# Kernel optimization log

Hardware: AMD Instinct MI355X
Metric: run time of the kernel (lower is better)

## Reference

```python
import jax, jax.numpy as jnp
import numpy as np

S, B, D, H = 2048, 2, 1024, 16
DK = D // H
SCALE = 1.0 / np.sqrt(DK)


def setup_inputs() -> dict:
    key = jax.random.key(0)
    ks = jax.random.split(key, 12)
    std = 1.0 / np.sqrt(D)
    inp = {
        "query": jax.random.normal(ks[0], (S, B, D), jnp.float32),
        "key": jax.random.normal(ks[1], (S, B, D), jnp.float32),
        "value": jax.random.normal(ks[2], (S, B, D), jnp.float32),
        # causal mask [S, S, 1]; mask[i, j] = 1 iff query i may attend key j
        "mask": jnp.tril(jnp.ones((S, S), jnp.bool_))[:, :, None],
        "Wq": jax.random.normal(ks[3], (D, D), jnp.float32) * std,
        "bq": jax.random.normal(ks[4], (D,), jnp.float32) * std,
        "Wk": jax.random.normal(ks[5], (D, D), jnp.float32) * std,
        "bk": jax.random.normal(ks[6], (D,), jnp.float32) * std,
        "Wv": jax.random.normal(ks[7], (D, D), jnp.float32) * std,
        "bv": jax.random.normal(ks[8], (D,), jnp.float32) * std,
        "Wo": jax.random.normal(ks[9], (D, D), jnp.float32) * std,
        "bo": jax.random.normal(ks[10], (D,), jnp.float32) * std,
    }
    return inp


def _proj(x, W, b):
    # nn.Linear: x @ W.T + b, then split into heads -> [S, B, H, DK]
    s, bsz, _ = x.shape
    y = jnp.einsum('sbd,ed->sbe', x, W) + b
    return y.reshape(s, bsz, H, DK)


def reference(query, key, value, mask, Wq, bq, Wk, bk, Wv, bv, Wo, bo):
    q = _proj(query, Wq, bq)   # [S,B,H,DK]
    k = _proj(key, Wk, bk)
    v = _proj(value, Wv, bv)
    scores = jnp.einsum('ibhd,jbhd->ijbh', q, k) * SCALE  # [S,S,B,H]
    m = mask[:, :, :, None]  # [S,S,1,1] or [S,S,B,1]
    scores = jnp.where(m, scores, jnp.float32(-1e9))
    attn = jax.nn.softmax(scores, axis=1)
    x = jnp.einsum('ijbh,jbhd->ibhd', attn, v)  # [S,B,H,DK]
    x = x.reshape(S, B, D)
    return jnp.einsum('sbd,ed->sbe', x, Wo) + bo
```

## Files before the change

### kernel.cpp

```cpp
#include <hip/hip_runtime.h>
#include <stdint.h>

#define S_LEN 2048
#define BATCH 2
#define DMODEL 1024
#define NHEAD 16
#define DHEAD 64
#define QSCALE 0.18033688011112042f

typedef float f32x4 __attribute__((ext_vector_type(4)));
typedef float f32x16 __attribute__((ext_vector_type(16)));
typedef __bf16 bf16x8 __attribute__((ext_vector_type(8)));

#if __has_builtin(__builtin_amdgcn_exp2f)
#define EXP2(x) __builtin_amdgcn_exp2f(x)
#else
#define EXP2(x) exp2f(x)
#endif

__device__ __forceinline__ unsigned short f2bf(float f) {
  union { float f; unsigned int u; } v;
  v.f = f;
  unsigned int u = v.u;
  return (unsigned short)((u + 0x7fffu + ((u >> 16) & 1u)) >> 16);
}

__device__ __forceinline__ unsigned pk2(float lo, float hi_) {
  union { __bf16 h[2]; unsigned u; } c;
  c.h[0] = (__bf16)lo; c.h[1] = (__bf16)hi_;
  return c.u;
}

__device__ __forceinline__ void gld16(const void* g, void* l) {
  __builtin_amdgcn_global_load_lds((__attribute__((address_space(1))) void*)(g),
                                   (__attribute__((address_space(3))) void*)(l),
                                   16, 0, 0);
}

__global__ void cvt_all_kernel(const float* __restrict__ q, const float* __restrict__ k,
                               const float* __restrict__ v, const float* __restrict__ wq,
                               const float* __restrict__ wk, const float* __restrict__ wv,
                               const float* __restrict__ wosrc, unsigned short* __restrict__ xp,
                               unsigned short* __restrict__ wp, unsigned short* __restrict__ wo) {
  const int b = blockIdx.x;
  const float* src;
  unsigned short* dst;
  if (b < 12288) {
    const int z = b >> 12;
    const int local = b & 4095;
    src = (z == 0 ? q : (z == 1 ? k : v)) + (size_t)local * 1024;
    dst = xp + (size_t)z * 4194304 + (size_t)local * 1024;
  } else {
    const int z = (b - 12288) >> 10;
    const int local = (b - 12288) & 1023;
    src = (z == 0 ? wq : (z == 1 ? wk : (z == 2 ? wv : wosrc))) + (size_t)local * 1024;
    dst = (z < 3 ? wp + (size_t)z * 1048576 : wo) + (size_t)local * 1024;
  }
  const int i = threadIdx.x * 4;
  const float4 val = *(const float4*)(src + i);
  ushort4 o;
  o.x = f2bf(val.x); o.y = f2bf(val.y); o.z = f2bf(val.z); o.w = f2bf(val.w);
  *(ushort4*)(dst + i) = o;
}

template <int MODE>
__global__ __launch_bounds__(256, 2) void gemm_bt(
    const unsigned short* __restrict__ Abase,
    const unsigned short* __restrict__ Wbase,
    const float* __restrict__ bias0, const float* __restrict__ bias1,
    const float* __restrict__ bias2,
    unsigned short* __restrict__ qw, unsigned short* __restrict__ kw,
    unsigned short* __restrict__ vtw, float* __restrict__ outp) {
  constexpr int M = S_LEN * BATCH;
  constexpr int N = DMODEL;
  constexpr int K = DMODEL;
  __shared__ unsigned short At[128 * 32];
  __shared__ unsigned short Bt[128 * 32];

  const int m0 = blockIdx.x * 128;
  const int n0 = blockIdx.y * 128;
  const int z = (MODE == 0) ? blockIdx.z : 0;
  const unsigned short* A = Abase + (size_t)z * M * K;
  const unsigned short* W = Wbase + (size_t)z * N * K;
  const float* bias = (z == 0 ? bias0 : (z == 1 ? bias1 : bias2));

  const int tid = threadIdx.x;
  const int w = tid >> 6, l = tid & 63;
  const int wr = w >> 1, wc = w & 1;
  const int lr = l & 15, lg = l >> 4;

  const int srow = tid >> 2;
  const int scol = (tid & 3) * 8;

  f32x4 acc[4][4] = {};

  for (int k0 = 0; k0 < K; k0 += 32) {
    {
      const unsigned short* ga0 = A + (size_t)(m0 + srow) * K + k0 + scol;
      const unsigned short* ga1 = A + (size_t)(m0 + 64 + srow) * K + k0 + scol;
      const unsigned short* gb0 = W + (size_t)(n0 + srow) * K + k0 + scol;
      const unsigned short* gb1 = W + (size_t)(n0 + 64 + srow) * K + k0 + scol;
      char* la = (char*)At + w * 1024;
      char* lb = (char*)Bt + w * 1024;
      gld16(ga0, la);
      gld16(ga1, la + 4096);
      gld16(gb0, lb);
      gld16(gb1, lb + 4096);
    }
    __syncthreads();
    bf16x8 af[4], bfr[4];
#pragma unroll
    for (int mt = 0; mt < 4; ++mt)
      af[mt] = *(const bf16x8*)&At[(wr * 64 + mt * 16 + lr) * 32 + lg * 8];
#pragma unroll
    for (int nt = 0; nt < 4; ++nt)
      bfr[nt] = *(const bf16x8*)&Bt[(wc * 64 + nt * 16 + lr) * 32 + lg * 8];
#pragma unroll
    for (int mt = 0; mt < 4; ++mt)
#pragma unroll
      for (int nt = 0; nt < 4; ++nt)
        acc[mt][nt] = __builtin_amdgcn_mfma_f32_16x16x32_bf16(af[mt], bfr[nt], acc[mt][nt], 0, 0, 0);
    __syncthreads();
  }

#pragma unroll
  for (int mt = 0; mt < 4; ++mt) {
#pragma unroll
    for (int nt = 0; nt < 4; ++nt) {
#pragma unroll
      for (int r = 0; r < 4; ++r) {
        const int gm = m0 + wr * 64 + mt * 16 + lg * 4 + r;
        const int gn = n0 + wc * 64 + nt * 16 + lr;
        float v = acc[mt][nt][r] + bias[gn];
        if (MODE == 1) {
          outp[(size_t)gm * N + gn] = v;
        } else {
          if (z == 0) v *= QSCALE;
          const int s = gm >> 1, bb = gm & 1;
          const int h = gn >> 6, dk = gn & 63;
          const int bh = bb * NHEAD + h;
          const unsigned short bv_ = f2bf(v);
          if (z == 0)
            qw[((size_t)bh * S_LEN + s) * DHEAD + dk] = bv_;
          else if (z == 1)
            kw[((size_t)bh * S_LEN + s) * DHEAD + dk] = bv_;
          else
            vtw[((size_t)bh * DHEAD + dk) * S_LEN + s] = bv_;
        }
      }
    }
  }
}

__global__ __launch_bounds__(256) void attn_kernel(
    const unsigned short* __restrict__ qw, const unsigned short* __restrict__ kw,
    const unsigned short* __restrict__ vtw, unsigned short* __restrict__ x2) {
  __shared__ unsigned short klds[2][8192];
  __shared__ unsigned short vlds[2][8192];
  __shared__ float mlscr[2][64][2];

  const int bh = blockIdx.x;
  const int xq = blockIdx.y;
  const int bb = bh >> 4, h = bh & 15;
  const int tid = threadIdx.x;
  const int w = tid >> 6, l = tid & 63;
  const int q5 = l & 31, hi = l >> 5;
  const int pair = w >> 1, wh = w & 1;

  const size_t qkbase = (size_t)bh * S_LEN * DHEAD;
  const size_t vbase = (size_t)bh * DHEAD * S_LEN;

  const int qtA = 31 - xq, qtB = xq;
  const int nA = qtA + 1, nB = qtB + 1;
  const int nsA = (nA + 1) >> 1;
  const int nsTot = nsA + ((nB + 1) >> 1);

  auto stage = [&](int kt0, int kt1, int b) {
#pragma unroll
    for (int r = 0; r < 4; ++r) {
      const int kt = (r >= 2) ? kt1 : kt0;
      const int idx = (r * 256 + tid) & 511;
      const int row = idx >> 3;
      const int sw = (idx & 7) ^ (row & 7);
      gld16(kw + qkbase + (size_t)(kt * 64 + row) * DHEAD + sw * 8,
            (char*)&klds[b][0] + r * 4096 + w * 1024);
      gld16(vtw + vbase + (size_t)row * S_LEN + kt * 64 + sw * 8,
            (char*)&vlds[b][0] + r * 4096 + w * 1024);
    }
  };

  int qt = qtA;
  int qrow = qt * 64 + wh * 32 + q5;
  bf16x8 qf[4];
#pragma unroll
  for (int d = 0; d < 4; ++d)
    qf[d] = *(const bf16x8*)&qw[qkbase + (size_t)qrow * DHEAD + d * 16 + hi * 8];

  f32x16 oacc0, oacc1;
#pragma unroll
  for (int r = 0; r < 16; ++r) { oacc0[r] = 0.f; oacc1[r] = 0.f; }
  float mrun = -1e30f, lrun = 0.f;

  stage(0, 1, 0);
  __syncthreads();

  for (int s = 0; s < nsTot; ++s) {
    const int cur = s & 1;
    if (s + 1 < nsTot) {
      int t0, lim;
      if (s + 1 < nsA) { t0 = 2 * (s + 1); lim = nA; }
      else { t0 = 2 * (s + 1 - nsA); lim = nB; }
      const int k1 = (t0 + 1 < lim) ? t0 + 1 : lim - 1;
      stage(t0, k1, cur ^ 1);
    }

    const bool phA = (s < nsA);
    const int myt = (phA ? 2 * s : 2 * (s - nsA)) + pair;
    const int lim = phA ? nA : nB;

    if (myt < lim) {
      const int kt = myt;
      const char* kb = (const char*)&klds[cur][0] + pair * 8192;
      const char* vb = (const char*)&vlds[cur][0] + pair * 8192;

      f32x16 scA, scB;
#pragma unroll
      for (int r = 0; r < 16; ++r) { scA[r] = 0.f; scB[r] = 0.f; }
      __builtin_amdgcn_s_setprio(1);
#pragma unroll
      for (int d = 0; d < 4; ++d) {
        const int ch = (2 * d + hi) ^ (q5 & 7);
        const bf16x8 kfA = *(const bf16x8*)(kb + q5 * 128 + ch * 16);
        const bf16x8 kfB = *(const bf16x8*)(kb + (32 + q5) * 128 + ch * 16);
        scA = __builtin_amdgcn_mfma_f32_32x32x16_bf16(kfA, qf[d], scA, 0, 0, 0);
        scB = __builtin_amdgcn_mfma_f32_32x32x16_bf16(kfB, qf[d], scB, 0, 0, 0);
      }
      __builtin_amdgcn_s_setprio(0);

      if (kt == qt) {
        const int qloc = wh * 32 + q5;
#pragma unroll
        for (int r = 0; r < 16; ++r) {
          const int kv = (r & 3) + 8 * (r >> 2) + 4 * hi;
          if (kv > qloc) scA[r] = -1e9f;
          if (kv + 32 > qloc) scB[r] = -1e9f;
        }
      }

      float mx[8];
#pragma unroll
      for (int j = 0; j < 8; ++j)
        mx[j] = fmaxf(fmaxf(scA[j], scA[j + 8]), fmaxf(scB[j], scB[j + 8]));
#pragma unroll
      for (int j = 0; j < 4; ++j) mx[j] = fmaxf(mx[j], mx[j + 4]);
      float tmax = fmaxf(fmaxf(mx[0], mx[1]), fmaxf(mx[2], mx[3]));
      tmax = fmaxf(tmax, __shfl_xor(tmax, 32, 64));
      const float mnew = fmaxf(mrun, tmax);
      const float resc = EXP2(mrun - mnew);
      mrun = mnew;
#pragma unroll
      for (int r = 0; r < 16; ++r) scA[r] = EXP2(scA[r] - mnew);
#pragma unroll
      for (int r = 0; r < 16; ++r) scB[r] = EXP2(scB[r] - mnew);
      float sm[8];
#pragma unroll
      for (int j = 0; j < 8; ++j)
        sm[j] = (scA[j] + scA[j + 8]) + (scB[j] + scB[j + 8]);
#pragma unroll
      for (int j = 0; j < 4; ++j) sm[j] += sm[j + 4];
      float rsum = (sm[0] + sm[1]) + (sm[2] + sm[3]);
      rsum += __shfl_xor(rsum, 32, 64);
      lrun = lrun * resc + rsum;
#pragma unroll
      for (int r = 0; r < 16; ++r) { oacc0[r] *= resc; oacc1[r] *= resc; }

      unsigned pk[2][8];
#pragma unroll
      for (int g = 0; g < 4; ++g) {
        pk[0][2 * g]     = pk2(scA[4 * g],     scA[4 * g + 1]);
        pk[0][2 * g + 1] = pk2(scA[4 * g + 2], scA[4 * g + 3]);
        pk[1][2 * g]     = pk2(scB[4 * g],     scB[4 * g + 1]);
        pk[1][2 * g + 1] = pk2(scB[4 * g + 2], scB[4 * g + 3]);
      }

#pragma unroll
      for (int t = 0; t < 4; ++t) {
        const int c = t >> 1, ks = t & 1;
        const unsigned o0 = pk[c][4 * ks + 0], o1 = pk[c][4 * ks + 1];
        const unsigned o2 = pk[c][4 * ks + 2], o3 = pk[c][4 * ks + 3];
        const unsigned ea = (unsigned)__shfl_xor((int)(hi ? o0 : o2), 32, 64);
        const unsigned eb = (unsigned)__shfl_xor((int)(hi ? o1 : o3), 32, 64);
        union { unsigned u[4]; bf16x8 v; } pb;
        pb.u[0] = hi ? ea : o0;
        pb.u[1] = hi ? eb : o1;
        pb.u[2] = hi ? o2 : ea;
        pb.u[3] = hi ? o3 : eb;
        const int vch = (2 * t + hi) ^ (q5 & 7);
        const bf16x8 vf0 = *(const bf16x8*)(vb + q5 * 128 + vch * 16);
        const bf16x8 vf1 = *(const bf16x8*)(vb + (32 + q5) * 128 + vch * 16);
        __builtin_amdgcn_s_setprio(1);
        oacc0 = __builtin_amdgcn_mfma_f32_32x32x16_bf16(vf0, pb.v, oacc0, 0, 0, 0);
        oacc1 = __builtin_amdgcn_mfma_f32_32x32x16_bf16(vf1, pb.v, oacc1, 0, 0, 0);
        __builtin_amdgcn_s_setprio(0);
      }
    }

    if (s == nsA - 1 || s == nsTot - 1) {
      __syncthreads();
      float* scr = (float*)&klds[cur][0];
      const int kx = l & 7;
      if (pair == 1) {
        f32x4* d4 = (f32x4*)(scr + (size_t)(wh * 64 + l) * 32);
#pragma unroll
        for (int c = 0; c < 4; ++c) {
          f32x4 ch_;
#pragma unroll
          for (int j = 0; j < 4; ++j) ch_[j] = oacc0[c * 4 + j];
          d4[c ^ kx] = ch_;
        }
#pragma unroll
        for (int c = 0; c < 4; ++c) {
          f32x4 ch_;
#pragma unroll
          for (int j = 0; j < 4; ++j) ch_[j] = oacc1[c * 4 + j];
          d4[(4 + c) ^ kx] = ch_;
        }
        mlscr[wh][l][0] = mrun;
        mlscr[wh][l][1] = lrun;
      }
      __syncthreads();
      if (pair == 0) {
        const f32x4* s4 = (const f32x4*)(scr + (size_t)(wh * 64 + l) * 32);
        const float m1 = mlscr[wh][l][0], l1 = mlscr[wh][l][1];
        const float ms = fmaxf(mrun, m1);
        const float a0 = EXP2(mrun - ms), a1 = EXP2(m1 - ms);
        const float lm = lrun * a0 + l1 * a1;
        const float invl = 1.0f / lm;
        const size_t obase = ((size_t)qrow * BATCH + bb) * DMODEL + h * DHEAD;
#pragma unroll
        for (int g = 0; g < 4; ++g) {
          const f32x4 c0 = s4[g ^ kx];
          const f32x4 c1 = s4[(4 + g) ^ kx];
          ushort4 s0, s1;
          s0.x = f2bf((oacc0[4 * g + 0] * a0 + c0[0] * a1) * invl);
          s0.y = f2bf((oacc0[4 * g + 1] * a0 + c0[1] * a1) * invl);
          s0.z = f2bf((oacc0[4 * g + 2] * a0 + c0[2] * a1) * invl);
          s0.w = f2bf((oacc0[4 * g + 3] * a0 + c0[3] * a1) * invl);
          s1.x = f2bf((oacc1[4 * g + 0] * a0 + c1[0] * a1) * invl);
          s1.y = f2bf((oacc1[4 * g + 1] * a0 + c1[1] * a1) * invl);
          s1.z = f2bf((oacc1[4 * g + 2] * a0 + c1[2] * a1) * invl);
          s1.w = f2bf((oacc1[4 * g + 3] * a0 + c1[3] * a1) * invl);
          const int d0 = 8 * g + 4 * hi;
          *(ushort4*)(x2 + obase + d0) = s0;
          *(ushort4*)(x2 + obase + 32 + d0) = s1;
        }
      }
      if (s == nsA - 1) {
        qt = qtB;
        qrow = qt * 64 + wh * 32 + q5;
#pragma unroll
        for (int d = 0; d < 4; ++d)
          qf[d] = *(const bf16x8*)&qw[qkbase + (size_t)qrow * DHEAD + d * 16 + hi * 8];
#pragma unroll
        for (int r = 0; r < 16; ++r) { oacc0[r] = 0.f; oacc1[r] = 0.f; }
        mrun = -1e30f;
        lrun = 0.f;
      }
    }
    __syncthreads();
  }
}

extern "C" void kernel_launch(void* const* d_in, const int* in_sizes, int n_in,
                              void* d_out, int out_size, void* d_ws, size_t ws_size,
                              hipStream_t stream) {
  (void)in_sizes; (void)n_in; (void)out_size;
  if (ws_size < (size_t)67108864) return;

  const float* query = (const float*)d_in[0];
  const float* key_  = (const float*)d_in[1];
  const float* value = (const float*)d_in[2];
  const float* Wq = (const float*)d_in[4];
  const float* bq = (const float*)d_in[5];
  const float* Wk = (const float*)d_in[6];
  const float* bk = (const float*)d_in[7];
  const float* Wv = (const float*)d_in[8];
  const float* bv = (const float*)d_in[9];
  const float* Wo = (const float*)d_in[10];
  const float* bo = (const float*)d_in[11];

  char* ws = (char*)d_ws;
  unsigned short* xp = (unsigned short*)(ws);
  unsigned short* wp = (unsigned short*)(ws + 25165824);
  unsigned short* wo = (unsigned short*)(ws + 31457280);
  unsigned short* qws = (unsigned short*)(ws + 33554432);
  unsigned short* kws = (unsigned short*)(ws + 41943040);
  unsigned short* vtw = (unsigned short*)(ws + 50331648);
  unsigned short* x2 = (unsigned short*)(ws + 58720256);

  cvt_all_kernel<<<16384, 256, 0, stream>>>(query, key_, value, Wq, Wk, Wv, Wo, xp, wp, wo);

  gemm_bt<0><<<dim3(32, 8, 3), 256, 0, stream>>>(xp, wp, bq, bk, bv, qws, kws, vtw, nullptr);
  attn_kernel<<<dim3(32, 16), 256, 0, stream>>>(qws, kws, vtw, x2);
  gemm_bt<1><<<dim3(32, 8, 1), 256, 0, stream>>>(x2, wo, bo, bo, bo, nullptr, nullptr, nullptr,
                                                 (float*)d_out);
}
```

Before: 131.6 us.

## Fuse fp32-to-bf16 input conversion into QKV GEMM, widen attention to 8 waves

Drops the separate conversion pass over the activations: the QKV projection GEMM now loads fp32 query, key and value directly, converts them to bf16 in registers and writes a padded LDS tile, prefetching the next K-slice. The attention kernel grows to 512 threads with four key-tile groups per step, a single LDS buffer restaged after each step, and a three-way partial merge at the end. It also adds a lazy softmax rescale that skips the max update when the new max stays within 8 of the running one, and switches EXP2 to exp2f. The fused conversion saves a full read-write pass over about 50 MB of activations, but the attention kernel loses its double buffering and now waits on the restage between steps.

```diff
diff --git a/kernel.cpp b/kernel.cpp
--- a/kernel.cpp
+++ b/kernel.cpp
@@ -11,12 +11,9 @@
 typedef float f32x4 __attribute__((ext_vector_type(4)));
 typedef float f32x16 __attribute__((ext_vector_type(16)));
 typedef __bf16 bf16x8 __attribute__((ext_vector_type(8)));
-
-#if __has_builtin(__builtin_amdgcn_exp2f)
-#define EXP2(x) __builtin_amdgcn_exp2f(x)
-#else
+typedef unsigned short u16x8 __attribute__((ext_vector_type(8)));
+
 #define EXP2(x) exp2f(x)
-#endif
 
 __device__ __forceinline__ unsigned short f2bf(float f) {
   union { float f; unsigned int u; } v;
@@ -37,25 +34,13 @@
                                    16, 0, 0);
 }
 
-__global__ void cvt_all_kernel(const float* __restrict__ q, const float* __restrict__ k,
-                               const float* __restrict__ v, const float* __restrict__ wq,
-                               const float* __restrict__ wk, const float* __restrict__ wv,
-                               const float* __restrict__ wosrc, unsigned short* __restrict__ xp,
-                               unsigned short* __restrict__ wp, unsigned short* __restrict__ wo) {
+__global__ void cvt_w_kernel(const float* __restrict__ wq, const float* __restrict__ wk,
+                             const float* __restrict__ wv, const float* __restrict__ wosrc,
+                             unsigned short* __restrict__ wp, unsigned short* __restrict__ wo) {
   const int b = blockIdx.x;
-  const float* src;
-  unsigned short* dst;
-  if (b < 12288) {
-    const int z = b >> 12;
-    const int local = b & 4095;
-    src = (z == 0 ? q : (z == 1 ? k : v)) + (size_t)local * 1024;
-    dst = xp + (size_t)z * 4194304 + (size_t)local * 1024;
-  } else {
-    const int z = (b - 12288) >> 10;
-    const int local = (b - 12288) & 1023;
-    src = (z == 0 ? wq : (z == 1 ? wk : (z == 2 ? wv : wosrc))) + (size_t)local * 1024;
-    dst = (z < 3 ? wp + (size_t)z * 1048576 : wo) + (size_t)local * 1024;
-  }
+  const int z = b >> 10, local = b & 1023;
+  const float* src = (z == 0 ? wq : (z == 1 ? wk : (z == 2 ? wv : wosrc))) + (size_t)local * 1024;
+  unsigned short* dst = (z < 3 ? wp + (size_t)z * 1048576 : wo) + (size_t)local * 1024;
   const int i = threadIdx.x * 4;
   const float4 val = *(const float4*)(src + i);
   ushort4 o;
@@ -65,22 +50,22 @@
 
 template <int MODE>
 __global__ __launch_bounds__(256, 2) void gemm_bt(
-    const unsigned short* __restrict__ Abase,
+    const float* __restrict__ Aq, const float* __restrict__ Akk, const float* __restrict__ Avv,
+    const unsigned short* __restrict__ Ab,
     const unsigned short* __restrict__ Wbase,
     const float* __restrict__ bias0, const float* __restrict__ bias1,
     const float* __restrict__ bias2,
     unsigned short* __restrict__ qw, unsigned short* __restrict__ kw,
     unsigned short* __restrict__ vtw, float* __restrict__ outp) {
-  constexpr int M = S_LEN * BATCH;
   constexpr int N = DMODEL;
   constexpr int K = DMODEL;
-  __shared__ unsigned short At[128 * 32];
+  constexpr int AST = (MODE == 0) ? 40 : 32;
+  __shared__ unsigned short At[128 * AST];
   __shared__ unsigned short Bt[128 * 32];
 
   const int m0 = blockIdx.x * 128;
   const int n0 = blockIdx.y * 128;
   const int z = (MODE == 0) ? blockIdx.z : 0;
-  const unsigned short* A = Abase + (size_t)z * M * K;
   const unsigned short* W = Wbase + (size_t)z * N * K;
   const float* bias = (z == 0 ? bias0 : (z == 1 ? bias1 : bias2));
 
@@ -92,26 +77,46 @@
   const int srow = tid >> 2;
   const int scol = (tid & 3) * 8;
 
+  const int arow = tid >> 1;
+  const int aks = (tid & 1) << 4;
+  const float* Af = (MODE == 0) ? (z == 0 ? Aq : (z == 1 ? Akk : Avv)) : nullptr;
+  const float* abase = (MODE == 0) ? (Af + (size_t)(m0 + arow) * K + aks) : nullptr;
+
+  float4 av[4];
+  if (MODE == 0) {
+#pragma unroll
+    for (int c = 0; c < 4; ++c) av[c] = *(const float4*)(abase + 4 * c);
+  }
+
   f32x4 acc[4][4] = {};
 
   for (int k0 = 0; k0 < K; k0 += 32) {
-    {
-      const unsigned short* ga0 = A + (size_t)(m0 + srow) * K + k0 + scol;
-      const unsigned short* ga1 = A + (size_t)(m0 + 64 + srow) * K + k0 + scol;
-      const unsigned short* gb0 = W + (size_t)(n0 + srow) * K + k0 + scol;
-      const unsigned short* gb1 = W + (size_t)(n0 + 64 + srow) * K + k0 + scol;
-      char* la = (char*)At + w * 1024;
-      char* lb = (char*)Bt + w * 1024;
-      gld16(ga0, la);
-      gld16(ga1, la + 4096);
-      gld16(gb0, lb);
-      gld16(gb1, lb + 4096);
-    }
+    if (k0) __syncthreads();
+    if (MODE == 0) {
+      union { __bf16 h[8]; u16x8 v; } c0, c1;
+#pragma unroll
+      for (int j = 0; j < 4; ++j) { c0.h[j] = (__bf16)av[0][j]; c0.h[4 + j] = (__bf16)av[1][j]; }
+#pragma unroll
+      for (int j = 0; j < 4; ++j) { c1.h[j] = (__bf16)av[2][j]; c1.h[4 + j] = (__bf16)av[3][j]; }
+      *(u16x8*)&At[arow * AST + aks] = c0.v;
+      *(u16x8*)&At[arow * AST + aks + 8] = c1.v;
+    } else {
+      gld16(Ab + (size_t)(m0 + srow) * K + k0 + scol, (char*)At + w * 1024);
+      gld16(Ab + (size_t)(m0 + 64 + srow) * K + k0 + scol, (char*)At + w * 1024 + 4096);
+    }
+    gld16(W + (size_t)(n0 + srow) * K + k0 + scol, (char*)Bt + w * 1024);
+    gld16(W + (size_t)(n0 + 64 + srow) * K + k0 + scol, (char*)Bt + w * 1024 + 4096);
     __syncthreads();
+
+    if (MODE == 0 && k0 + 32 < K) {
+#pragma unroll
+      for (int c = 0; c < 4; ++c) av[c] = *(const float4*)(abase + k0 + 32 + 4 * c);
+    }
+
     bf16x8 af[4], bfr[4];
 #pragma unroll
     for (int mt = 0; mt < 4; ++mt)
-      af[mt] = *(const bf16x8*)&At[(wr * 64 + mt * 16 + lr) * 32 + lg * 8];
+      af[mt] = *(const bf16x8*)&At[(wr * 64 + mt * 16 + lr) * AST + lg * 8];
 #pragma unroll
     for (int nt = 0; nt < 4; ++nt)
       bfr[nt] = *(const bf16x8*)&Bt[(wc * 64 + nt * 16 + lr) * 32 + lg * 8];
@@ -120,7 +125,6 @@
 #pragma unroll
       for (int nt = 0; nt < 4; ++nt)
         acc[mt][nt] = __builtin_amdgcn_mfma_f32_16x16x32_bf16(af[mt], bfr[nt], acc[mt][nt], 0, 0, 0);
-    __syncthreads();
   }
 
 #pragma unroll
@@ -152,12 +156,11 @@
   }
 }
 
-__global__ __launch_bounds__(256) void attn_kernel(
+__global__ __launch_bounds__(512) void attn_kernel(
     const unsigned short* __restrict__ qw, const unsigned short* __restrict__ kw,
     const unsigned short* __restrict__ vtw, unsigned short* __restrict__ x2) {
-  __shared__ unsigned short klds[2][8192];
-  __shared__ unsigned short vlds[2][8192];
-  __shared__ float mlscr[2][64][2];
+  __shared__ unsigned short lds_all[32768];
+  __shared__ float mlscr[3][2][64][2];
 
   const int bh = blockIdx.x;
   const int xq = blockIdx.y;
@@ -165,27 +168,29 @@
   const int tid = threadIdx.x;
   const int w = tid >> 6, l = tid & 63;
   const int q5 = l & 31, hi = l >> 5;
-  const int pair = w >> 1, wh = w & 1;
+  const int quar = w >> 1, wh = w & 1;
 
   const size_t qkbase = (size_t)bh * S_LEN * DHEAD;
   const size_t vbase = (size_t)bh * DHEAD * S_LEN;
 
   const int qtA = 31 - xq, qtB = xq;
   const int nA = qtA + 1, nB = qtB + 1;
-  const int nsA = (nA + 1) >> 1;
-  const int nsTot = nsA + ((nB + 1) >> 1);
-
-  auto stage = [&](int kt0, int kt1, int b) {
+  const int sA = (nA + 3) >> 2;
+  const int sTot = sA + ((nB + 3) >> 2);
+
+  auto stage = [&](int t0, int lim) {
 #pragma unroll
     for (int r = 0; r < 4; ++r) {
-      const int kt = (r >= 2) ? kt1 : kt0;
-      const int idx = (r * 256 + tid) & 511;
-      const int row = idx >> 3;
-      const int sw = (idx & 7) ^ (row & 7);
-      gld16(kw + qkbase + (size_t)(kt * 64 + row) * DHEAD + sw * 8,
-            (char*)&klds[b][0] + r * 4096 + w * 1024);
-      gld16(vtw + vbase + (size_t)row * S_LEN + kt * 64 + sw * 8,
-            (char*)&vlds[b][0] + r * 4096 + w * 1024);
+      const int g = w * 4 + r;
+      const int ti = g >> 3;
+      const int row = ((g & 7) << 3) + (l >> 3);
+      const int ch = (l & 7) ^ (row & 7);
+      int t = t0 + ti;
+      if (t >= lim) t = lim - 1;
+      gld16(kw + qkbase + (size_t)(t * 64 + row) * DHEAD + ch * 8,
+            (char*)lds_all + g * 1024);
+      gld16(vtw + vbase + (size_t)row * S_LEN + t * 64 + ch * 8,
+            (char*)lds_all + 32768 + g * 1024);
     }
   };
 
@@ -201,27 +206,19 @@
   for (int r = 0; r < 16; ++r) { oacc0[r] = 0.f; oacc1[r] = 0.f; }
   float mrun = -1e30f, lrun = 0.f;
 
-  stage(0, 1, 0);
+  stage(0, nA);
   __syncthreads();
 
-  for (int s = 0; s < nsTot; ++s) {
-    const int cur = s & 1;
-    if (s + 1 < nsTot) {
-      int t0, lim;
-      if (s + 1 < nsA) { t0 = 2 * (s + 1); lim = nA; }
-      else { t0 = 2 * (s + 1 - nsA); lim = nB; }
-      const int k1 = (t0 + 1 < lim) ? t0 + 1 : lim - 1;
-      stage(t0, k1, cur ^ 1);
-    }
-
-    const bool phA = (s < nsA);
-    const int myt = (phA ? 2 * s : 2 * (s - nsA)) + pair;
+  const char* kb = (const char*)lds_all + quar * 8192;
+  const char* vb = (const char*)lds_all + 32768 + quar * 8192;
+
+  for (int s = 0; s < sTot; ++s) {
+    const bool phA = (s < sA);
+    const int myt = (phA ? 4 * s : 4 * (s - sA)) + quar;
     const int lim = phA ? nA : nB;
 
     if (myt < lim) {
       const int kt = myt;
-      const char* kb = (const char*)&klds[cur][0] + pair * 8192;
-      const char* vb = (const char*)&vlds[cur][0] + pair * 8192;
 
       f32x16 scA, scB;
 #pragma unroll
@@ -255,13 +252,18 @@
       for (int j = 0; j < 4; ++j) mx[j] = fmaxf(mx[j], mx[j + 4]);
       float tmax = fmaxf(fmaxf(mx[0], mx[1]), fmaxf(mx[2], mx[3]));
       tmax = fmaxf(tmax, __shfl_xor(tmax, 32, 64));
-      const float mnew = fmaxf(mrun, tmax);
-      const float resc = EXP2(mrun - mnew);
-      mrun = mnew;
-#pragma unroll
-      for (int r = 0; r < 16; ++r) scA[r] = EXP2(scA[r] - mnew);
-#pragma unroll
-      for (int r = 0; r < 16; ++r) scB[r] = EXP2(scB[r] - mnew);
+      if (!__all(tmax <= mrun + 8.0f)) {
+        const float mnew = fmaxf(mrun, tmax);
+        const float resc = EXP2(mrun - mnew);
+        mrun = mnew;
+        lrun *= resc;
+#pragma unroll
+        for (int r = 0; r < 16; ++r) { oacc0[r] *= resc; oacc1[r] *= resc; }
+      }
+#pragma unroll
+      for (int r = 0; r < 16; ++r) scA[r] = EXP2(scA[r] - mrun);
+#pragma unroll
+      for (int r = 0; r < 16; ++r) scB[r] = EXP2(scB[r] - mrun);
       float sm[8];
 #pragma unroll
       for (int j = 0; j < 8; ++j)
@@ -270,9 +272,7 @@
       for (int j = 0; j < 4; ++j) sm[j] += sm[j + 4];
       float rsum = (sm[0] + sm[1]) + (sm[2] + sm[3]);
       rsum += __shfl_xor(rsum, 32, 64);
-      lrun = lrun * resc + rsum;
-#pragma unroll
-      for (int r = 0; r < 16; ++r) { oacc0[r] *= resc; oacc1[r] *= resc; }
+      lrun += rsum;
 
       unsigned pk[2][8];
 #pragma unroll
@@ -305,12 +305,12 @@
       }
     }
 
-    if (s == nsA - 1 || s == nsTot - 1) {
+    if (s == sA - 1 || s == sTot - 1) {
       __syncthreads();
-      float* scr = (float*)&klds[cur][0];
+      float* scr = (float*)lds_all;
       const int kx = l & 7;
-      if (pair == 1) {
-        f32x4* d4 = (f32x4*)(scr + (size_t)(wh * 64 + l) * 32);
+      if (quar != 0) {
+        f32x4* d4 = (f32x4*)(scr + (size_t)(((quar - 1) * 2 + wh) * 64 + l) * 32);
 #pragma unroll
         for (int c = 0; c < 4; ++c) {
           f32x4 ch_;
@@ -325,37 +325,51 @@
           for (int j = 0; j < 4; ++j) ch_[j] = oacc1[c * 4 + j];
           d4[(4 + c) ^ kx] = ch_;
         }
-        mlscr[wh][l][0] = mrun;
-        mlscr[wh][l][1] = lrun;
+        mlscr[quar - 1][wh][l][0] = mrun;
+        mlscr[quar - 1][wh][l][1] = lrun;
       }
       __syncthreads();
-      if (pair == 0) {
-        const f32x4* s4 = (const f32x4*)(scr + (size_t)(wh * 64 + l) * 32);
-        const float m1 = mlscr[wh][l][0], l1 = mlscr[wh][l][1];
-        const float ms = fmaxf(mrun, m1);
-        const float a0 = EXP2(mrun - ms), a1 = EXP2(m1 - ms);
-        const float lm = lrun * a0 + l1 * a1;
+      if (quar == 0) {
+        float ms = mrun, lm = lrun;
+        f32x16 a0 = oacc0, a1 = oacc1;
+#pragma unroll
+        for (int p = 1; p <= 3; ++p) {
+          const f32x4* s4 = (const f32x4*)(scr + (size_t)(((p - 1) * 2 + wh) * 64 + l) * 32);
+          const float mp = mlscr[p - 1][wh][l][0], lp = mlscr[p - 1][wh][l][1];
+          const float mn = fmaxf(ms, mp);
+          const float c0 = EXP2(ms - mn), c1 = EXP2(mp - mn);
+#pragma unroll
+          for (int g = 0; g < 4; ++g) {
+            const f32x4 p0 = s4[g ^ kx];
+            const f32x4 p1 = s4[(4 + g) ^ kx];
+#pragma unroll
+            for (int j = 0; j < 4; ++j) {
+              a0[4 * g + j] = a0[4 * g + j] * c0 + p0[j] * c1;
+              a1[4 * g + j] = a1[4 * g + j] * c0 + p1[j] * c1;
+            }
+          }
+          lm = lm * c0 + lp * c1;
+          ms = mn;
+        }
         const float invl = 1.0f / lm;
         const size_t obase = ((size_t)qrow * BATCH + bb) * DMODEL + h * DHEAD;
 #pragma unroll
         for (int g = 0; g < 4; ++g) {
-          const f32x4 c0 = s4[g ^ kx];
-          const f32x4 c1 = s4[(4 + g) ^ kx];
+          const int d0 = 8 * g + 4 * hi;
           ushort4 s0, s1;
-          s0.x = f2bf((oacc0[4 * g + 0] * a0 + c0[0] * a1) * invl);
-          s0.y = f2bf((oacc0[4 * g + 1] * a0 + c0[1] * a1) * invl);
-          s0.z = f2bf((oacc0[4 * g + 2] * a0 + c0[2] * a1) * invl);
-          s0.w = f2bf((oacc0[4 * g + 3] * a0 + c0[3] * a1) * invl);
-          s1.x = f2bf((oacc1[4 * g + 0] * a0 + c1[0] * a1) * invl);
-          s1.y = f2bf((oacc1[4 * g + 1] * a0 + c1[1] * a1) * invl);
-          s1.z = f2bf((oacc1[4 * g + 2] * a0 + c1[2] * a1) * invl);
-          s1.w = f2bf((oacc1[4 * g + 3] * a0 + c1[3] * a1) * invl);
-          const int d0 = 8 * g + 4 * hi;
+          s0.x = f2bf(a0[4 * g + 0] * invl);
+          s0.y = f2bf(a0[4 * g + 1] * invl);
+          s0.z = f2bf(a0[4 * g + 2] * invl);
+          s0.w = f2bf(a0[4 * g + 3] * invl);
+          s1.x = f2bf(a1[4 * g + 0] * invl);
+          s1.y = f2bf(a1[4 * g + 1] * invl);
+          s1.z = f2bf(a1[4 * g + 2] * invl);
+          s1.w = f2bf(a1[4 * g + 3] * invl);
           *(ushort4*)(x2 + obase + d0) = s0;
           *(ushort4*)(x2 + obase + 32 + d0) = s1;
         }
       }
-      if (s == nsA - 1) {
+      if (s == sA - 1) {
         qt = qtB;
         qrow = qt * 64 + wh * 32 + q5;
 #pragma unroll
@@ -366,6 +380,14 @@
         mrun = -1e30f;
         lrun = 0.f;
       }
+    }
+
+    __syncthreads();
+    if (s + 1 < sTot) {
+      int t0, lim2;
+      if (s + 1 < sA) { t0 = 4 * (s + 1); lim2 = nA; }
+      else { t0 = 4 * (s + 1 - sA); lim2 = nB; }
+      stage(t0, lim2);
     }
     __syncthreads();
   }
@@ -390,18 +412,19 @@
   const float* bo = (const float*)d_in[11];
 
   char* ws = (char*)d_ws;
-  unsigned short* xp = (unsigned short*)(ws);
-  unsigned short* wp = (unsigned short*)(ws + 25165824);
-  unsigned short* wo = (unsigned short*)(ws + 31457280);
-  unsigned short* qws = (unsigned short*)(ws + 33554432);
-  unsigned short* kws = (unsigned short*)(ws + 41943040);
-  unsigned short* vtw = (unsigned short*)(ws + 50331648);
-  unsigned short* x2 = (unsigned short*)(ws + 58720256);
-
-  cvt_all_kernel<<<16384, 256, 0, stream>>>(query, key_, value, Wq, Wk, Wv, Wo, xp, wp, wo);
-
-  gemm_bt<0><<<dim3(32, 8, 3), 256, 0, stream>>>(xp, wp, bq, bk, bv, qws, kws, vtw, nullptr);
-  attn_kernel<<<dim3(32, 16), 256, 0, stream>>>(qws, kws, vtw, x2);
-  gemm_bt<1><<<dim3(32, 8, 1), 256, 0, stream>>>(x2, wo, bo, bo, bo, nullptr, nullptr, nullptr,
+  unsigned short* wp  = (unsigned short*)(ws);
+  unsigned short* wo  = (unsigned short*)(ws + 6291456);
+  unsigned short* qws = (unsigned short*)(ws + 8388608);
+  unsigned short* kws = (unsigned short*)(ws + 16777216);
+  unsigned short* vtw = (unsigned short*)(ws + 25165824);
+  unsigned short* x2  = (unsigned short*)(ws + 33554432);
+
+  cvt_w_kernel<<<4096, 256, 0, stream>>>(Wq, Wk, Wv, Wo, wp, wo);
+
+  gemm_bt<0><<<dim3(32, 8, 3), 256, 0, stream>>>(query, key_, value, nullptr, wp,
+                                                 bq, bk, bv, qws, kws, vtw, nullptr);
+  attn_kernel<<<dim3(32, 16), 512, 0, stream>>>(qws, kws, vtw, x2);
+  gemm_bt<1><<<dim3(32, 8, 1), 256, 0, stream>>>(nullptr, nullptr, nullptr, x2, wo,
+                                                 bo, bo, bo, nullptr, nullptr, nullptr,
                                                  (float*)d_out);
 }
```

Measured after the change: 141.0 us. 1.07x slower.
